# Performance work log

Measured on AMD Instinct MI355X. Metric: run time of the kernel, lower is better.

Reference implementation:

```python
import jax, jax.numpy as jnp
import numpy as np

B, T, N, IN = 16, 12, 2048, 1
HID, E_DIM, CHEB, HOR = 64, 10, 2, 12


def setup_inputs() -> dict:
    key = jax.random.key(0)
    ks = jax.random.split(key, 12)
    s = 0.1  # param scale to keep gates unsaturated
    return {
        "source": jax.random.normal(ks[0], (B, T, N, IN), jnp.float32),
        "node_embeddings": jax.random.normal(ks[1], (N, E_DIM), jnp.float32),
        "Wg0": jax.random.normal(ks[2], (E_DIM, CHEB, IN + HID, 2 * HID), jnp.float32) * s,
        "bg0": jax.random.normal(ks[3], (E_DIM, 2 * HID), jnp.float32) * s,
        "Wu0": jax.random.normal(ks[4], (E_DIM, CHEB, IN + HID, HID), jnp.float32) * s,
        "bu0": jax.random.normal(ks[5], (E_DIM, HID), jnp.float32) * s,
        "Wg1": jax.random.normal(ks[6], (E_DIM, CHEB, HID + HID, 2 * HID), jnp.float32) * s,
        "bg1": jax.random.normal(ks[7], (E_DIM, 2 * HID), jnp.float32) * s,
        "Wu1": jax.random.normal(ks[8], (E_DIM, CHEB, HID + HID, HID), jnp.float32) * s,
        "bu1": jax.random.normal(ks[9], (E_DIM, HID), jnp.float32) * s,
        "conv_w": jax.random.normal(ks[10], (HOR, HID), jnp.float32) * s,
        "conv_b": jax.random.normal(ks[11], (HOR,), jnp.float32) * s,
    }


def _cheb_supports(E, cheb_k):
    # softmax(relu(E E^T)) row-normalized adaptive adjacency + Chebyshev recursion
    S = jax.nn.softmax(jax.nn.relu(E @ E.T), axis=1)
    sup = [jnp.eye(E.shape[0], dtype=S.dtype), S]
    for _ in range(2, cheb_k):
        sup.append(2.0 * S @ sup[-1] - sup[-2])
    return jnp.stack(sup, axis=0)  # (K, N, N)


def _gcn(x, supports, weights, bias):
    # x: (B,N,C); weights: (N,K,C,O); bias: (N,O)
    x_g = jnp.einsum('knm,bmc->bnkc', supports, x)
    return jnp.einsum('bnki,nkio->bno', x_g, weights) + bias


def _layer(x_seq, supports, E, Wg, bg, Wu, bu, hid):
    # precompute node-adaptive weights/biases (constant across time)
    wg = jnp.einsum('nd,dkio->nkio', E, Wg)
    bgv = E @ bg
    wu = jnp.einsum('nd,dkio->nkio', E, Wu)
    buv = E @ bu

    def step(state, x_t):
        inp = jnp.concatenate([x_t, state], axis=-1)
        zr = jax.nn.sigmoid(_gcn(inp, supports, wg, bgv))
        z, r = jnp.split(zr, 2, axis=-1)
        cand = jnp.concatenate([x_t, z * state], axis=-1)
        hc = jnp.tanh(_gcn(cand, supports, wu, buv))
        h = r * state + (1.0 - r) * hc
        return h, h

    init = jnp.zeros((x_seq.shape[0], x_seq.shape[2], hid), dtype=x_seq.dtype)
    _, hs = jax.lax.scan(step, init, jnp.swapaxes(x_seq, 0, 1))  # (T,B,N,H)
    return jnp.swapaxes(hs, 0, 1)  # (B,T,N,H)


def reference(source, node_embeddings, Wg0, bg0, Wu0, bu0, Wg1, bg1, Wu1, bu1, conv_w, conv_b):
    supports = _cheb_supports(node_embeddings, CHEB)
    h1 = _layer(source, supports, node_embeddings, Wg0, bg0, Wu0, bu0, HID)
    h2 = _layer(h1, supports, node_embeddings, Wg1, bg1, Wu1, bu1, HID)
    last = h2[:, -1]  # (B,N,HID)
    # Conv2d(1, horizon, kernel=(1,HID)) on (B,1,N,HID) == per-node linear over HID
    out = jnp.einsum('bnc,hc->bhn', last, conv_w) + conv_b[None, :, None]
    return out  # (B, horizon, N)
```

## Files before the change

kernel.cpp:

```cpp
#include <hip/hip_runtime.h>
#include <hip/hip_bf16.h>


#define B_    16
#define T_    12
#define N_    2048
#define HID_  64
#define ED_   10
#define HOR_  12
#define BH    (B_*HID_)
#define BT    (B_*T_)
#define SL_   (N_*BH)

typedef __hip_bfloat16 bf16;
typedef __attribute__((ext_vector_type(8))) short short8;
typedef __attribute__((ext_vector_type(4))) float floatx4;

__device__ int            g_flag[64];
__device__ float          g_Ein[N_*ED_];
__device__ float          g_cwf[HOR_*HID_];
__device__ float          g_cbf[HOR_ + 4];
__device__ unsigned short g_Shi[N_*N_];
__device__ unsigned short g_Slo[N_*N_];
__device__ float          g_Wg0F[ED_*128*160];
__device__ float          g_Wu0F[ED_*64*160];
__device__ float          g_Wg1F[ED_*128*256];
__device__ float          g_Wu1F[ED_*64*256];
__device__ unsigned short g_Wg0H[ED_*128*160];
__device__ unsigned short g_Wu0H[ED_*64*160];
__device__ unsigned short g_Wg1H[ED_*128*256];
__device__ unsigned short g_Wu1H[ED_*64*256];
__device__ float          g_bgv0[N_*128];
__device__ float          g_buv0[N_*64];
__device__ float          g_bgv1[N_*128];
__device__ float          g_buv1[N_*64];
__device__ float          g_srcf[BT*N_];
__device__ unsigned short g_srcHi[BT*N_];
__device__ unsigned short g_srcLo[BT*N_];
__device__ float          g_Sx0[N_*BT];
__device__ float          g_h[2*SL_];
__device__ float          g_Sh[2*SL_];
__device__ float          g_zh[SL_];
__device__ float          g_rbuf[SL_];
__device__ unsigned short g_tmpTh[SL_];
__device__ unsigned short g_tmpTl[SL_];
__device__ unsigned short g_h2Th[SL_];
__device__ unsigned short g_h2Tl[SL_];

__device__ __forceinline__ float b2f(bf16 x){ return __bfloat162float(x); }
__device__ __forceinline__ bf16  f2b(float x){ return __float2bfloat16(x); }
__device__ __forceinline__ float bits2f(unsigned u) {
  union { float f; unsigned i; } c; c.i = u << 16; return c.f;
}
__device__ __forceinline__ float ldin(const void* p, size_t i, int isbf) {
  return isbf ? b2f(((const bf16*)p)[i]) : ((const float*)p)[i];
}
__device__ __forceinline__ void fma4(float4& a, float s, const float4& b) {
  a.x += s*b.x; a.y += s*b.y; a.z += s*b.z; a.w += s*b.w;
}

__global__ void k_detect(const void* __restrict__ E) {
  __shared__ int cnt;
  if (threadIdx.x == 0) cnt = 0;
  __syncthreads();
  const unsigned* w = (const unsigned*)E;
  int c = 0;
  for (int i = threadIdx.x; i < 4096; i += 256) {
    const unsigned e = (w[i] >> 7) & 0xFFu;
    if (e >= 0x6Eu && e <= 0x86u) ++c;
  }
  atomicAdd(&cnt, c);
  __syncthreads();
  if (threadIdx.x == 0) g_flag[0] = (cnt > 2048) ? 1 : 0;
}

__global__ void k_castE(const void* __restrict__ E) {
  const int i = blockIdx.x*256 + threadIdx.x;
  if (i < N_*ED_) g_Ein[i] = ldin(E, i, g_flag[0]);
}
__global__ void k_castsrc(const void* __restrict__ src) {
  const int i = blockIdx.x*256 + threadIdx.x;
  if (i < B_*T_*N_) g_srcf[i] = ldin(src, i, g_flag[0]);
}
__global__ void k_castc(const void* __restrict__ cw, const void* __restrict__ cb) {
  const int i = blockIdx.x*256 + threadIdx.x;
  const int f = g_flag[0];
  if (i < HOR_*HID_) g_cwf[i] = ldin(cw, i, f);
  if (i < HOR_)      g_cbf[i] = ldin(cb, i, f);
}

__global__ __launch_bounds__(256) void k_softmax_S() {
  bf16* Sh = (bf16*)g_Shi;
  bf16* Sl = (bf16*)g_Slo;
  const int n = blockIdx.x, tid = threadIdx.x;
  __shared__ float er[ED_];
  __shared__ float red[4];
  if (tid < ED_) er[tid] = g_Ein[n*ED_ + tid];
  __syncthreads();
  float e[ED_];
#pragma unroll
  for (int d = 0; d < ED_; ++d) e[d] = er[d];
  float v[8];
  float mx = 0.f;
#pragma unroll
  for (int j = 0; j < 8; ++j) {
    const int m = tid + j*256;
    float dot = 0.f;
#pragma unroll
    for (int d = 0; d < ED_; ++d) dot += e[d]*g_Ein[m*ED_ + d];
    v[j] = fmaxf(dot, 0.f);
    mx = fmaxf(mx, v[j]);
  }
  for (int o = 32; o; o >>= 1) mx = fmaxf(mx, __shfl_xor(mx, o, 64));
  if ((tid & 63) == 0) red[tid >> 6] = mx;
  __syncthreads();
  mx = fmaxf(fmaxf(red[0], red[1]), fmaxf(red[2], red[3]));
  __syncthreads();
  float sum = 0.f;
#pragma unroll
  for (int j = 0; j < 8; ++j) { v[j] = __expf(v[j] - mx); sum += v[j]; }
  for (int o = 32; o; o >>= 1) sum += __shfl_xor(sum, o, 64);
  if ((tid & 63) == 0) red[tid >> 6] = sum;
  __syncthreads();
  sum = red[0] + red[1] + red[2] + red[3];
  const float inv = 1.f / sum;
#pragma unroll
  for (int j = 0; j < 8; ++j) {
    const float sv = v[j]*inv;
    const size_t idx = (size_t)n*N_ + tid + j*256;
    const bf16 h = f2b(sv);
    Sh[idx] = h;
    Sl[idx] = f2b(sv - b2f(h));
  }
}

__global__ void k_splitSrc() {
  const int i = blockIdx.x*256 + threadIdx.x;
  if (i < BT*N_) {
    const float v = g_srcf[i];
    const bf16 h = f2b(v);
    ((bf16*)g_srcHi)[i] = h;
    ((bf16*)g_srcLo)[i] = f2b(v - b2f(h));
  }
}

__global__ __launch_bounds__(256) void k_trsp(int xsel, int dsel) {
  const float* X = (xsel == 0) ? g_h : (xsel == 1) ? (g_h + SL_) : g_zh;
  bf16* Th = (bf16*)((dsel == 0) ? g_tmpTh : g_h2Th);
  bf16* Tl = (bf16*)((dsel == 0) ? g_tmpTl : g_h2Tl);
  const int n0 = blockIdx.x * 64;
  const int c0 = blockIdx.y * 64;
  __shared__ float t[64][68];
  const int tid = threadIdx.x;
  {
    const int r = tid >> 2, q4 = (tid & 3) * 16;
    const float4* src = (const float4*)(X + (size_t)(n0 + r)*BH + c0 + q4);
#pragma unroll
    for (int u = 0; u < 4; ++u)
      *(float4*)&t[r][q4 + u*4] = src[u];
  }
  __syncthreads();
  {
    const int c = tid >> 2, sg = (tid & 3) * 16;
    bf16 hb[16], lb[16];
#pragma unroll
    for (int i = 0; i < 16; ++i) {
      const float v = t[sg + i][c];
      const bf16 h = f2b(v);
      hb[i] = h;
      lb[i] = f2b(v - b2f(h));
    }
    bf16* dh = Th + (size_t)(c0 + c)*N_ + n0 + sg;
    bf16* dl = Tl + (size_t)(c0 + c)*N_ + n0 + sg;
    *(uint4*)dh       = *(uint4*)&hb[0];
    *(uint4*)(dh + 8) = *(uint4*)&hb[8];
    *(uint4*)dl       = *(uint4*)&lb[0];
    *(uint4*)(dl + 8) = *(uint4*)&lb[8];
  }
}

template<int LAYER>
__global__ __launch_bounds__(256) void k_prepP(const void* __restrict__ Wb,
                                               int KIin, int KIP, int O,
                                               int wsel) {
  float* PF = (wsel == 0) ? g_Wg0F : (wsel == 1) ? g_Wu0F
            : (wsel == 2) ? g_Wg1F : g_Wu1F;
  bf16* PH = (bf16*)((wsel == 0) ? g_Wg0H : (wsel == 1) ? g_Wu0H
            : (wsel == 2) ? g_Wg1H : g_Wu1H);
  const int idx = blockIdx.x*256 + threadIdx.x;
  if (idx >= ED_*O*KIP) return;
  const int d = idx / (O*KIP), rem = idx - d*O*KIP;
  const int o = rem / KIP, kp = rem - o*KIP;
  int cheb, i; bool valid;
  if (LAYER == 0) {
    cheb = (kp >= 80) ? 1 : 0;
    const int local = kp - cheb*80;
    if (local < 64)       { i = local + 1; valid = true; }
    else if (local == 64) { i = 0;         valid = true; }
    else                  { i = 0;         valid = false; }
  } else {
    cheb = kp >> 7; i = kp & 127; valid = true;
  }
  float v = 0.f;
  if (valid) v = ldin(Wb, (size_t)((d*2 + cheb)*KIin + i)*O + o, g_flag[0]);
  const int kg = kp >> 2, e = kp & 3;
  const size_t pi = ((size_t)(o*(KIP/4) + kg)*ED_ + d)*4 + e;
  PF[pi] = v;
  PH[pi] = f2b(v);
}

__global__ __launch_bounds__(128) void k_matb(const void* __restrict__ bb,
                                              int O, int osel) {
  float* outv = (osel == 0) ? g_bgv0 : (osel == 1) ? g_buv0
              : (osel == 2) ? g_bgv1 : g_buv1;
  const int n = blockIdx.x, tid = threadIdx.x;
  if (tid >= O) return;
  const int f = g_flag[0];
  float acc = 0.f;
#pragma unroll
  for (int d = 0; d < ED_; ++d) acc += g_Ein[n*ED_ + d]*ldin(bb, d*O + tid, f);
  outv[n*O + tid] = acc;
}

__global__ __launch_bounds__(256) void k_gemmM(int x1, int c1, int ldc1,
                                               int x2, int c2, int ldc2,
                                               int split) {
  const bf16* Sh = (const bf16*)g_Shi;
  const bf16* Sl = (const bf16*)g_Slo;
  const int bm = blockIdx.x * 128;
  int bc = blockIdx.y * 64;
  int xs = x1, cs = c1, ldc = ldc1;
  if (bc >= split) { xs = x2; cs = c2; ldc = ldc2; bc -= split; }
  const bf16* Xh = (const bf16*)((xs == 0) ? g_tmpTh : (xs == 1) ? g_h2Th : g_srcHi);
  const bf16* Xl = (const bf16*)((xs == 0) ? g_tmpTl : (xs == 1) ? g_h2Tl : g_srcLo);
  float* C = (cs == 0) ? g_Sh : (cs == 1) ? (g_Sh + SL_) : g_Sx0;

  __shared__ __align__(16) bf16 Ah[128][72];
  __shared__ __align__(16) bf16 Al[128][72];
  __shared__ __align__(16) bf16 Bh[64][72];
  __shared__ __align__(16) bf16 Bl[64][72];
  const int tid = threadIdx.x;
  const int wave = tid >> 6, lane = tid & 63, q = lane >> 4, ln = lane & 15;
  const int wm = wave >> 1, wn = wave & 1;
  const int srow = tid >> 3, scol = (tid & 7) * 8;

  floatx4 acc[4][2];
#pragma unroll
  for (int mt = 0; mt < 4; ++mt)
#pragma unroll
    for (int nt = 0; nt < 2; ++nt) acc[mt][nt] = (floatx4){0.f,0.f,0.f,0.f};

  for (int mk = 0; mk < N_; mk += 64) {
#pragma unroll
    for (int i = 0; i < 4; ++i) {
      const int r = i*32 + srow;
      *(uint4*)&Ah[r][scol] = *(const uint4*)(Sh + (size_t)(bm + r)*N_ + mk + scol);
      *(uint4*)&Al[r][scol] = *(const uint4*)(Sl + (size_t)(bm + r)*N_ + mk + scol);
    }
#pragma unroll
    for (int i = 0; i < 2; ++i) {
      const int r = i*32 + srow;
      *(uint4*)&Bh[r][scol] = *(const uint4*)(Xh + (size_t)(bc + r)*N_ + mk + scol);
      *(uint4*)&Bl[r][scol] = *(const uint4*)(Xl + (size_t)(bc + r)*N_ + mk + scol);
    }
    __syncthreads();
#pragma unroll
    for (int ks = 0; ks < 64; ks += 32) {
      short8 ah[4], al[4], bh[2], bl[2];
#pragma unroll
      for (int mt = 0; mt < 4; ++mt) {
        ah[mt] = *(const short8*)&Ah[wm*64 + mt*16 + ln][ks + q*8];
        al[mt] = *(const short8*)&Al[wm*64 + mt*16 + ln][ks + q*8];
      }
#pragma unroll
      for (int nt = 0; nt < 2; ++nt) {
        bh[nt] = *(const short8*)&Bh[wn*32 + nt*16 + ln][ks + q*8];
        bl[nt] = *(const short8*)&Bl[wn*32 + nt*16 + ln][ks + q*8];
      }
#pragma unroll
      for (int mt = 0; mt < 4; ++mt)
#pragma unroll
        for (int nt = 0; nt < 2; ++nt) {
          acc[mt][nt] = __builtin_amdgcn_mfma_f32_16x16x32_bf16(ah[mt], bh[nt], acc[mt][nt], 0, 0, 0);
          acc[mt][nt] = __builtin_amdgcn_mfma_f32_16x16x32_bf16(al[mt], bh[nt], acc[mt][nt], 0, 0, 0);
          acc[mt][nt] = __builtin_amdgcn_mfma_f32_16x16x32_bf16(ah[mt], bl[nt], acc[mt][nt], 0, 0, 0);
        }
    }
    __syncthreads();
  }
#pragma unroll
  for (int mt = 0; mt < 4; ++mt)
#pragma unroll
    for (int nt = 0; nt < 2; ++nt)
#pragma unroll
      for (int r = 0; r < 4; ++r)
        C[(size_t)(bm + wm*64 + mt*16 + q*4 + r)*ldc + bc + wn*32 + nt*16 + ln] =
            acc[mt][nt][r];
}

template<int LAYER, int KIP, int KIPP>
__device__ __forceinline__ void build4(float (*xg)[KIPP],
                                       const float* p0, const float* p1,
                                       const float* p2, const float* p3,
                                       int n, int t, int tid) {
  constexpr int NQ = KIP/4;
  for (int idx = tid; idx < B_*NQ; idx += 256) {
    const int b = idx / NQ, k = (idx - b*NQ) * 4;
    float4 v = make_float4(0.f, 0.f, 0.f, 0.f);
    if (LAYER == 1) {
      const float* rg = (k < 64) ? p0 : (k < 128) ? p1 : (k < 192) ? p2 : p3;
      v = *(const float4*)(rg + (size_t)n*BH + b*64 + (k & 63));
    } else {
      if (k < 64)        v = *(const float4*)(p0 + (size_t)n*BH + b*64 + k);
      else if (k == 64)  v.x = p1[(size_t)(b*T_ + t)*N_ + n];
      else if (k >= 80 && k < 144)
                         v = *(const float4*)(p2 + (size_t)n*BH + b*64 + (k - 80));
      else if (k == 144) v.x = p3[(size_t)n*BT + b*T_ + t];
    }
    *(float4*)&xg[b][k] = v;
  }
}

template<int KIP>
__device__ __forceinline__ void merge_p2(const float* __restrict__ PF,
                                         const bf16* __restrict__ PH,
                                         const float* el0, const float* el1,
                                         int o, int kg, int isbf,
                                         float4& a0, float4& a1) {
  const size_t gbase = (size_t)(o*(KIP/4) + kg)*(ED_*4);
  if (isbf) {
    const uint4* g = (const uint4*)(PH + gbase);
#pragma unroll
    for (int i = 0; i < 5; ++i) {
      const uint4 w = g[i];
      const float f0 = bits2f(w.x & 0xFFFFu), f1 = bits2f(w.x >> 16);
      const float f2 = bits2f(w.y & 0xFFFFu), f3 = bits2f(w.y >> 16);
      const float f4 = bits2f(w.z & 0xFFFFu), f5 = bits2f(w.z >> 16);
      const float f6 = bits2f(w.w & 0xFFFFu), f7 = bits2f(w.w >> 16);
      const float e00 = el0[2*i], e01 = el0[2*i + 1];
      const float e10 = el1[2*i], e11 = el1[2*i + 1];
      a0.x += e00*f0; a0.y += e00*f1; a0.z += e00*f2; a0.w += e00*f3;
      a0.x += e01*f4; a0.y += e01*f5; a0.z += e01*f6; a0.w += e01*f7;
      a1.x += e10*f0; a1.y += e10*f1; a1.z += e10*f2; a1.w += e10*f3;
      a1.x += e11*f4; a1.y += e11*f5; a1.z += e11*f6; a1.w += e11*f7;
    }
  } else {
    const float4* g = (const float4*)(PF + gbase);
#pragma unroll
    for (int d = 0; d < ED_; ++d) {
      const float4 w = g[d];
      fma4(a0, el0[d], w);
      fma4(a1, el1[d], w);
    }
  }
}

template<int LAYER, int KIP>
__global__ __launch_bounds__(256, 2) void k_gateW2(int t) {
  constexpr int KIPP = KIP + 4;
  constexpr int O = 128;
  const float* PF = (LAYER == 0) ? g_Wg0F : g_Wg1F;
  const bf16*  PH = (const bf16*)((LAYER == 0) ? g_Wg0H : g_Wg1H);
  const float* bgv = (LAYER == 0) ? g_bgv0 : g_bgv1;
  const float* p0 = g_h;
  const float* p1 = (LAYER == 0) ? g_srcf : (g_h + SL_);
  const float* p2 = g_Sh;
  const float* p3 = (LAYER == 0) ? g_Sx0 : (g_Sh + SL_);
  const float* hstate = (LAYER == 0) ? g_h : (g_h + SL_);
  const int n0 = blockIdx.x, n1 = blockIdx.x + N_/2, tid = threadIdx.x;
  __shared__ float xg[2][B_][KIPP];
  __shared__ float wm[2][O][36];
  __shared__ float es[2][ED_];
  if (tid < ED_) es[0][tid] = g_Ein[n0*ED_ + tid];
  if (tid >= 32 && tid < 32 + ED_) es[1][tid - 32] = g_Ein[n1*ED_ + (tid - 32)];
  build4<LAYER, KIP, KIPP>(xg[0], p0, p1, p2, p3, n0, t, tid);
  build4<LAYER, KIP, KIPP>(xg[1], p0, p1, p2, p3, n1, t, tid);
  __syncthreads();
  const int isbf = g_flag[0];
  float el0[ED_], el1[ED_];
#pragma unroll
  for (int d = 0; d < ED_; ++d) { el0[d] = es[0][d]; el1[d] = es[1][d]; }

  const int b = tid >> 4, q = tid & 15;
  float ac0[8], ac1[8];
#pragma unroll
  for (int j = 0; j < 8; ++j) { ac0[j] = 0.f; ac1[j] = 0.f; }

  for (int k0 = 0; k0 < KIP; k0 += 32) {
#pragma unroll
    for (int i = 0; i < O*8/256; ++i) {
      const int idx = tid + i*256;
      const int o = idx >> 3, kq = idx & 7;
      float4 a0 = make_float4(0.f, 0.f, 0.f, 0.f);
      float4 a1 = make_float4(0.f, 0.f, 0.f, 0.f);
      merge_p2<KIP>(PF, PH, el0, el1, o, (k0 >> 2) + kq, isbf, a0, a1);
      *(float4*)&wm[0][o][kq*4] = a0;
      *(float4*)&wm[1][o][kq*4] = a1;
    }
    __syncthreads();
#pragma unroll
    for (int kq = 0; kq < 8; ++kq) {
      const float4 xv0 = *(const float4*)&xg[0][b][k0 + kq*4];
      const float4 xv1 = *(const float4*)&xg[1][b][k0 + kq*4];
#pragma unroll
      for (int j = 0; j < 8; ++j) {
        const float4 w0 = *(const float4*)&wm[0][q + 16*j][kq*4];
        const float4 w1 = *(const float4*)&wm[1][q + 16*j][kq*4];
        ac0[j] += xv0.x*w0.x + xv0.y*w0.y + xv0.z*w0.z + xv0.w*w0.w;
        ac1[j] += xv1.x*w1.x + xv1.y*w1.y + xv1.z*w1.z + xv1.w*w1.w;
      }
    }
    __syncthreads();
  }
#pragma unroll
  for (int j = 0; j < 8; ++j) {
    const int o = q + 16*j;
    {
      float s = ac0[j] + bgv[n0*128 + o];
      s = 1.f/(1.f + __expf(-s));
      if (o < HID_) {
        g_zh[(size_t)n0*BH + b*64 + o] = s*hstate[(size_t)n0*BH + b*64 + o];
      } else {
        g_rbuf[(size_t)n0*BH + b*64 + (o - HID_)] = s;
      }
    }
    {
      float s = ac1[j] + bgv[n1*128 + o];
      s = 1.f/(1.f + __expf(-s));
      if (o < HID_) {
        g_zh[(size_t)n1*BH + b*64 + o] = s*hstate[(size_t)n1*BH + b*64 + o];
      } else {
        g_rbuf[(size_t)n1*BH + b*64 + (o - HID_)] = s;
      }
    }
  }
}

template<int LAYER, int KIP>
__global__ __launch_bounds__(256, 2) void k_candW2f(int t) {
  constexpr int KIPP = KIP + 4;
  constexpr int O = 64;
  const float* PF = (LAYER == 0) ? g_Wu0F : g_Wu1F;
  const bf16*  PH = (const bf16*)((LAYER == 0) ? g_Wu0H : g_Wu1H);
  const float* buv = (LAYER == 0) ? g_buv0 : g_buv1;
  const float* p0 = (LAYER == 0) ? g_zh : g_h;
  const float* p1 = (LAYER == 0) ? g_srcf : g_zh;
  const float* p2 = (LAYER == 0) ? (g_Sh + SL_) : g_Sh;
  const float* p3 = (LAYER == 0) ? g_Sx0 : (g_Sh + SL_);
  float* hstate = (LAYER == 0) ? g_h : (g_h + SL_);
  const int n0 = blockIdx.x, n1 = blockIdx.x + N_/2, tid = threadIdx.x;
  __shared__ float xg[2][B_][KIPP];
  __shared__ float wm[2][O][36];
  __shared__ float es[2][ED_];
  if (tid < ED_) es[0][tid] = g_Ein[n0*ED_ + tid];
  if (tid >= 32 && tid < 32 + ED_) es[1][tid - 32] = g_Ein[n1*ED_ + (tid - 32)];
  build4<LAYER, KIP, KIPP>(xg[0], p0, p1, p2, p3, n0, t, tid);
  build4<LAYER, KIP, KIPP>(xg[1], p0, p1, p2, p3, n1, t, tid);
  __syncthreads();
  const int isbf = g_flag[0];
  float el0[ED_], el1[ED_];
#pragma unroll
  for (int d = 0; d < ED_; ++d) { el0[d] = es[0][d]; el1[d] = es[1][d]; }

  const int b = tid >> 4, q = tid & 15;
  float ac0[4], ac1[4];
#pragma unroll
  for (int j = 0; j < 4; ++j) { ac0[j] = 0.f; ac1[j] = 0.f; }

  for (int k0 = 0; k0 < KIP; k0 += 32) {
#pragma unroll
    for (int i = 0; i < O*8/256; ++i) {
      const int idx = tid + i*256;
      const int o = idx >> 3, kq = idx & 7;
      float4 a0 = make_float4(0.f, 0.f, 0.f, 0.f);
      float4 a1 = make_float4(0.f, 0.f, 0.f, 0.f);
      merge_p2<KIP>(PF, PH, el0, el1, o, (k0 >> 2) + kq, isbf, a0, a1);
      *(float4*)&wm[0][o][kq*4] = a0;
      *(float4*)&wm[1][o][kq*4] = a1;
    }
    __syncthreads();
#pragma unroll
    for (int kq = 0; kq < 8; ++kq) {
      const float4 xv0 = *(const float4*)&xg[0][b][k0 + kq*4];
      const float4 xv1 = *(const float4*)&xg[1][b][k0 + kq*4];
#pragma unroll
      for (int j = 0; j < 4; ++j) {
        const float4 w0 = *(const float4*)&wm[0][q + 16*j][kq*4];
        const float4 w1 = *(const float4*)&wm[1][q + 16*j][kq*4];
        ac0[j] += xv0.x*w0.x + xv0.y*w0.y + xv0.z*w0.z + xv0.w*w0.w;
        ac1[j] += xv1.x*w1.x + xv1.y*w1.y + xv1.z*w1.z + xv1.w*w1.w;
      }
    }
    __syncthreads();
  }
#pragma unroll
  for (int j = 0; j < 4; ++j) {
    const int o = q + 16*j;
    {
      const float hc = tanhf(ac0[j] + buv[n0*64 + o]);
      const float rr = g_rbuf[(size_t)n0*BH + b*64 + o];
      const float hold = hstate[(size_t)n0*BH + b*64 + o];
      hstate[(size_t)n0*BH + b*64 + o] = rr*hold + (1.f - rr)*hc;
    }
    {
      const float hc = tanhf(ac1[j] + buv[n1*64 + o]);
      const float rr = g_rbuf[(size_t)n1*BH + b*64 + o];
      const float hold = hstate[(size_t)n1*BH + b*64 + o];
      hstate[(size_t)n1*BH + b*64 + o] = rr*hold + (1.f - rr)*hc;
    }
  }
}

__global__ void k_zero_f(int sel) {
  float* p = (sel == 0) ? g_h : g_Sh;
  const int i = blockIdx.x*256 + threadIdx.x;
  if (i < 2*SL_) p[i] = 0.f;
}

__global__ __launch_bounds__(256) void k_conv(void* __restrict__ out) {
  const float* h2 = g_h + SL_;
  const int n = blockIdx.x, tid = threadIdx.x;
  __shared__ float hs[BH];
  for (int i = tid; i < BH; i += 256) hs[i] = h2[(size_t)n*BH + i];
  __syncthreads();
  const int isbf = g_flag[0];
  for (int i = tid; i < B_*HOR_; i += 256) {
    const int b = i / HOR_, hor = i - b*HOR_;
    float acc = g_cbf[hor];
#pragma unroll
    for (int c = 0; c < HID_; ++c) acc += hs[b*HID_ + c]*g_cwf[hor*HID_ + c];
    const size_t oi = (size_t)(b*HOR_ + hor)*N_ + n;
    if (isbf) ((bf16*)out)[oi] = f2b(acc);
    else      ((float*)out)[oi] = acc;
  }
}

extern "C" void kernel_launch(void* const* d_in, const int* in_sizes, int n_in,
                              void* d_out, int out_size, void* d_ws, size_t ws_size,
                              hipStream_t stream) {
  (void)out_size; (void)d_ws; (void)ws_size;

  static const long long cnt[12] = {
    393216,
    20480,
    166400,
    1280,
    83200,
    640,
    327680,
    1280,
    163840,
    640,
    768,
    12
  };
  const void* in[12];
  bool ok = (n_in == 12) && (in_sizes != nullptr) && (d_in != nullptr);
  if (ok) {
    long long mx = 0;
    for (int i = 0; i < 12; ++i) if ((long long)in_sizes[i] > mx) mx = in_sizes[i];
    long long scale = mx / 393216LL;
    if (scale != 1 && scale != 2 && scale != 4) ok = false;
    if (ok && scale*393216LL != mx) ok = false;
    bool used[12] = {false,false,false,false,false,false,false,false,false,false,false,false};
    for (int k = 0; k < 12 && ok; ++k) {
      int found = -1;
      for (int i = 0; i < 12; ++i)
        if (!used[i] && (long long)in_sizes[i] == cnt[k]*scale) { found = i; break; }
      if (found < 0) ok = false;
      else { used[found] = true; in[k] = d_in[found]; }
    }
  }
  if (!ok) for (int k = 0; k < 12; ++k) in[k] = d_in[k];

  const void* src = in[0];
  const void* E   = in[1];
  const void* Wg0 = in[2];
  const void* bg0 = in[3];
  const void* Wu0 = in[4];
  const void* bu0 = in[5];
  const void* Wg1 = in[6];
  const void* bg1 = in[7];
  const void* Wu1 = in[8];
  const void* bu1 = in[9];
  const void* cw  = in[10];
  const void* cb  = in[11];

  auto cdiv = [](int a, int b) { return (a + b - 1) / b; };

  k_detect<<<dim3(1), 256, 0, stream>>>(E);

  k_castE  <<<dim3(cdiv(N_*ED_, 256)), 256, 0, stream>>>(E);
  k_castsrc<<<dim3(cdiv(BT*N_, 256)),  256, 0, stream>>>(src);
  k_castc  <<<dim3(cdiv(HOR_*HID_, 256)), 256, 0, stream>>>(cw, cb);
  k_prepP<0><<<dim3(cdiv(ED_*128*160, 256)), 256, 0, stream>>>(Wg0, 65, 160, 128, 0);
  k_prepP<0><<<dim3(cdiv(ED_*64*160,  256)), 256, 0, stream>>>(Wu0, 65, 160, 64, 1);
  k_prepP<1><<<dim3(cdiv(ED_*128*256, 256)), 256, 0, stream>>>(Wg1, 128, 256, 128, 2);
  k_prepP<1><<<dim3(cdiv(ED_*64*256,  256)), 256, 0, stream>>>(Wu1, 128, 256, 64, 3);
  k_matb<<<dim3(N_), 128, 0, stream>>>(bg0, 128, 0);
  k_matb<<<dim3(N_), 128, 0, stream>>>(bu0, 64,  1);
  k_matb<<<dim3(N_), 128, 0, stream>>>(bg1, 128, 2);
  k_matb<<<dim3(N_), 128, 0, stream>>>(bu1, 64,  3);
  k_softmax_S<<<dim3(N_), 256, 0, stream>>>();
  k_splitSrc<<<dim3(cdiv(BT*N_, 256)), 256, 0, stream>>>();

  k_gemmM<<<dim3(N_/128, BT/64), 256, 0, stream>>>(2, 2, BT, 2, 2, BT, 1 << 30);

  k_zero_f<<<dim3((2*SL_ + 255)/256), 256, 0, stream>>>(0);
  k_zero_f<<<dim3((2*SL_ + 255)/256), 256, 0, stream>>>(1);

  k_gateW2<0,160><<<dim3(N_/2), 256, 0, stream>>>(0);
  k_candW2f<0,160><<<dim3(N_/2), 256, 0, stream>>>(0);
  k_trsp<<<dim3(N_/64, BH/64), 256, 0, stream>>>(0, 0);
  k_gemmM<<<dim3(N_/128, BH/64), 256, 0, stream>>>(0, 0, BH, 0, 0, BH, 1 << 30);
  k_gateW2<1,256><<<dim3(N_/2), 256, 0, stream>>>(0);
  k_candW2f<1,256><<<dim3(N_/2), 256, 0, stream>>>(0);
  k_trsp<<<dim3(N_/64, BH/64), 256, 0, stream>>>(1, 1);

  for (int t = 1; t < T_; ++t) {
    k_gateW2<0,160><<<dim3(N_/2), 256, 0, stream>>>(t);
    k_trsp<<<dim3(N_/64, BH/64), 256, 0, stream>>>(2, 0);
    k_gemmM<<<dim3(N_/128, BH/64), 256, 0, stream>>>(0, 1, BH, 0, 1, BH, 1 << 30);
    k_candW2f<0,160><<<dim3(N_/2), 256, 0, stream>>>(t);
    k_trsp<<<dim3(N_/64, BH/64), 256, 0, stream>>>(0, 0);
    k_gemmM<<<dim3(N_/128, 2*BH/64), 256, 0, stream>>>(0, 0, BH, 1, 1, BH, BH);
    k_gateW2<1,256><<<dim3(N_/2), 256, 0, stream>>>(t);
    k_trsp<<<dim3(N_/64, BH/64), 256, 0, stream>>>(2, 0);
    k_gemmM<<<dim3(N_/128, BH/64), 256, 0, stream>>>(0, 1, BH, 0, 1, BH, 1 << 30);
    k_candW2f<1,256><<<dim3(N_/2), 256, 0, stream>>>(t);
    k_trsp<<<dim3(N_/64, BH/64), 256, 0, stream>>>(1, 1);
  }

  k_conv<<<dim3(N_), 256, 0, stream>>>(d_out);
}
```

Measured before the change: 6.704 ms.

## Precompute per-node merged weights once instead of re-merging every timestep

Adds k_merge kernels that materialize the node-adaptive weights (E·W) for all nodes into large fp32 global buffers before the recurrence. The gate and candidate kernels then stream these precomputed weights instead of recomputing the 10-term embedding contraction at every timestep, and each block now handles one node instead of two. This trades repeated ALU work for much higher memory traffic, reading roughly 130 MB of weights per timestep, and adds about the same amount of global storage.

```diff
diff --git a/kernel.cpp b/kernel.cpp
--- a/kernel.cpp
+++ b/kernel.cpp
@@ -46,6 +46,10 @@
 __device__ unsigned short g_tmpTl[SL_];
 __device__ unsigned short g_h2Th[SL_];
 __device__ unsigned short g_h2Tl[SL_];
+__device__ float          g_Wg0M[(size_t)N_*128*160];
+__device__ float          g_Wu0M[(size_t)N_*64*160];
+__device__ float          g_Wg1M[(size_t)N_*128*256];
+__device__ float          g_Wu1M[(size_t)N_*64*256];
 
 __device__ __forceinline__ float b2f(bf16 x){ return __bfloat162float(x); }
 __device__ __forceinline__ bf16  f2b(float x){ return __float2bfloat16(x); }
@@ -222,6 +226,55 @@
   outv[n*O + tid] = acc;
 }
 
+template<int KIP>
+__device__ __forceinline__ float4 merge_p(const float* __restrict__ PF,
+                                          const bf16* __restrict__ PH,
+                                          const float* el, int o, int kg,
+                                          int isbf) {
+  float4 a4 = make_float4(0.f, 0.f, 0.f, 0.f);
+  const size_t gbase = (size_t)(o*(KIP/4) + kg)*(ED_*4);
+  if (isbf) {
+    const uint4* g = (const uint4*)(PH + gbase);
+#pragma unroll
+    for (int i = 0; i < 5; ++i) {
+      const uint4 w = g[i];
+      const float e0 = el[2*i], e1 = el[2*i + 1];
+      a4.x += e0*bits2f(w.x & 0xFFFFu); a4.y += e0*bits2f(w.x >> 16);
+      a4.z += e0*bits2f(w.y & 0xFFFFu); a4.w += e0*bits2f(w.y >> 16);
+      a4.x += e1*bits2f(w.z & 0xFFFFu); a4.y += e1*bits2f(w.z >> 16);
+      a4.z += e1*bits2f(w.w & 0xFFFFu); a4.w += e1*bits2f(w.w >> 16);
+    }
+  } else {
+    const float4* g = (const float4*)(PF + gbase);
+#pragma unroll
+    for (int d = 0; d < ED_; ++d)
+      fma4(a4, el[d], g[d]);
+  }
+  return a4;
+}
+
+template<int KIP>
+__global__ __launch_bounds__(256) void k_merge(int O, int wsel) {
+  const float* PF = (wsel == 0) ? g_Wg0F : (wsel == 1) ? g_Wu0F
+                  : (wsel == 2) ? g_Wg1F : g_Wu1F;
+  const bf16* PH = (const bf16*)((wsel == 0) ? g_Wg0H : (wsel == 1) ? g_Wu0H
+                  : (wsel == 2) ? g_Wg1H : g_Wu1H);
+  float* WM = (wsel == 0) ? g_Wg0M : (wsel == 1) ? g_Wu0M
+            : (wsel == 2) ? g_Wg1M : g_Wu1M;
+  const int n = blockIdx.x;
+  const int idx = blockIdx.y*256 + threadIdx.x;
+  __shared__ float es[ED_];
+  if (threadIdx.x < ED_) es[threadIdx.x] = g_Ein[n*ED_ + threadIdx.x];
+  __syncthreads();
+  if (idx >= O*(KIP/4)) return;
+  const int o = idx / (KIP/4), kg = idx - o*(KIP/4);
+  float el[ED_];
+#pragma unroll
+  for (int d = 0; d < ED_; ++d) el[d] = es[d];
+  const float4 a4 = merge_p<KIP>(PF, PH, el, o, kg, g_flag[0]);
+  *(float4*)&WM[((size_t)n*O + o)*KIP + kg*4] = a4;
+}
+
 __global__ __launch_bounds__(256) void k_gemmM(int x1, int c1, int ldc1,
                                                int x2, int c2, int ldc2,
                                                int split) {
@@ -321,93 +374,44 @@
   }
 }
 
-template<int KIP>
-__device__ __forceinline__ void merge_p2(const float* __restrict__ PF,
-                                         const bf16* __restrict__ PH,
-                                         const float* el0, const float* el1,
-                                         int o, int kg, int isbf,
-                                         float4& a0, float4& a1) {
-  const size_t gbase = (size_t)(o*(KIP/4) + kg)*(ED_*4);
-  if (isbf) {
-    const uint4* g = (const uint4*)(PH + gbase);
-#pragma unroll
-    for (int i = 0; i < 5; ++i) {
-      const uint4 w = g[i];
-      const float f0 = bits2f(w.x & 0xFFFFu), f1 = bits2f(w.x >> 16);
-      const float f2 = bits2f(w.y & 0xFFFFu), f3 = bits2f(w.y >> 16);
-      const float f4 = bits2f(w.z & 0xFFFFu), f5 = bits2f(w.z >> 16);
-      const float f6 = bits2f(w.w & 0xFFFFu), f7 = bits2f(w.w >> 16);
-      const float e00 = el0[2*i], e01 = el0[2*i + 1];
-      const float e10 = el1[2*i], e11 = el1[2*i + 1];
-      a0.x += e00*f0; a0.y += e00*f1; a0.z += e00*f2; a0.w += e00*f3;
-      a0.x += e01*f4; a0.y += e01*f5; a0.z += e01*f6; a0.w += e01*f7;
-      a1.x += e10*f0; a1.y += e10*f1; a1.z += e10*f2; a1.w += e10*f3;
-      a1.x += e11*f4; a1.y += e11*f5; a1.z += e11*f6; a1.w += e11*f7;
-    }
-  } else {
-    const float4* g = (const float4*)(PF + gbase);
-#pragma unroll
-    for (int d = 0; d < ED_; ++d) {
-      const float4 w = g[d];
-      fma4(a0, el0[d], w);
-      fma4(a1, el1[d], w);
-    }
-  }
-}
-
 template<int LAYER, int KIP>
-__global__ __launch_bounds__(256, 2) void k_gateW2(int t) {
+__global__ __launch_bounds__(256, 2) void k_gateWpm(int t) {
   constexpr int KIPP = KIP + 4;
   constexpr int O = 128;
-  const float* PF = (LAYER == 0) ? g_Wg0F : g_Wg1F;
-  const bf16*  PH = (const bf16*)((LAYER == 0) ? g_Wg0H : g_Wg1H);
+  const float* WM = (LAYER == 0) ? g_Wg0M : g_Wg1M;
   const float* bgv = (LAYER == 0) ? g_bgv0 : g_bgv1;
   const float* p0 = g_h;
   const float* p1 = (LAYER == 0) ? g_srcf : (g_h + SL_);
   const float* p2 = g_Sh;
   const float* p3 = (LAYER == 0) ? g_Sx0 : (g_Sh + SL_);
   const float* hstate = (LAYER == 0) ? g_h : (g_h + SL_);
-  const int n0 = blockIdx.x, n1 = blockIdx.x + N_/2, tid = threadIdx.x;
-  __shared__ float xg[2][B_][KIPP];
-  __shared__ float wm[2][O][36];
-  __shared__ float es[2][ED_];
-  if (tid < ED_) es[0][tid] = g_Ein[n0*ED_ + tid];
-  if (tid >= 32 && tid < 32 + ED_) es[1][tid - 32] = g_Ein[n1*ED_ + (tid - 32)];
-  build4<LAYER, KIP, KIPP>(xg[0], p0, p1, p2, p3, n0, t, tid);
-  build4<LAYER, KIP, KIPP>(xg[1], p0, p1, p2, p3, n1, t, tid);
-  __syncthreads();
-  const int isbf = g_flag[0];
-  float el0[ED_], el1[ED_];
-#pragma unroll
-  for (int d = 0; d < ED_; ++d) { el0[d] = es[0][d]; el1[d] = es[1][d]; }
-
+  const int n = blockIdx.x, tid = threadIdx.x;
+  __shared__ float xg[B_][KIPP];
+  __shared__ float wm[O][36];
+  build4<LAYER, KIP, KIPP>(xg, p0, p1, p2, p3, n, t, tid);
+
+  const float* WMn = WM + (size_t)n*O*KIP;
   const int b = tid >> 4, q = tid & 15;
-  float ac0[8], ac1[8];
-#pragma unroll
-  for (int j = 0; j < 8; ++j) { ac0[j] = 0.f; ac1[j] = 0.f; }
+  float acc[8];
+#pragma unroll
+  for (int j = 0; j < 8; ++j) acc[j] = 0.f;
 
   for (int k0 = 0; k0 < KIP; k0 += 32) {
 #pragma unroll
     for (int i = 0; i < O*8/256; ++i) {
       const int idx = tid + i*256;
       const int o = idx >> 3, kq = idx & 7;
-      float4 a0 = make_float4(0.f, 0.f, 0.f, 0.f);
-      float4 a1 = make_float4(0.f, 0.f, 0.f, 0.f);
-      merge_p2<KIP>(PF, PH, el0, el1, o, (k0 >> 2) + kq, isbf, a0, a1);
-      *(float4*)&wm[0][o][kq*4] = a0;
-      *(float4*)&wm[1][o][kq*4] = a1;
+      *(float4*)&wm[o][kq*4] =
+          *(const float4*)(WMn + (size_t)o*KIP + k0 + kq*4);
     }
     __syncthreads();
 #pragma unroll
     for (int kq = 0; kq < 8; ++kq) {
-      const float4 xv0 = *(const float4*)&xg[0][b][k0 + kq*4];
-      const float4 xv1 = *(const float4*)&xg[1][b][k0 + kq*4];
+      const float4 xv = *(const float4*)&xg[b][k0 + kq*4];
 #pragma unroll
       for (int j = 0; j < 8; ++j) {
-        const float4 w0 = *(const float4*)&wm[0][q + 16*j][kq*4];
-        const float4 w1 = *(const float4*)&wm[1][q + 16*j][kq*4];
-        ac0[j] += xv0.x*w0.x + xv0.y*w0.y + xv0.z*w0.z + xv0.w*w0.w;
-        ac1[j] += xv1.x*w1.x + xv1.y*w1.y + xv1.z*w1.z + xv1.w*w1.w;
+        const float4 wv = *(const float4*)&wm[q + 16*j][kq*4];
+        acc[j] += xv.x*wv.x + xv.y*wv.y + xv.z*wv.z + xv.w*wv.w;
       }
     }
     __syncthreads();
@@ -415,80 +419,54 @@
 #pragma unroll
   for (int j = 0; j < 8; ++j) {
     const int o = q + 16*j;
-    {
-      float s = ac0[j] + bgv[n0*128 + o];
-      s = 1.f/(1.f + __expf(-s));
-      if (o < HID_) {
-        g_zh[(size_t)n0*BH + b*64 + o] = s*hstate[(size_t)n0*BH + b*64 + o];
-      } else {
-        g_rbuf[(size_t)n0*BH + b*64 + (o - HID_)] = s;
-      }
-    }
-    {
-      float s = ac1[j] + bgv[n1*128 + o];
-      s = 1.f/(1.f + __expf(-s));
-      if (o < HID_) {
-        g_zh[(size_t)n1*BH + b*64 + o] = s*hstate[(size_t)n1*BH + b*64 + o];
-      } else {
-        g_rbuf[(size_t)n1*BH + b*64 + (o - HID_)] = s;
-      }
+    float s = acc[j] + bgv[n*128 + o];
+    s = 1.f/(1.f + __expf(-s));
+    if (o < HID_) {
+      g_zh[(size_t)n*BH + b*64 + o] = s*hstate[(size_t)n*BH + b*64 + o];
+    } else {
+      g_rbuf[(size_t)n*BH + b*64 + (o - HID_)] = s;
     }
   }
 }
 
 template<int LAYER, int KIP>
-__global__ __launch_bounds__(256, 2) void k_candW2f(int t) {
+__global__ __launch_bounds__(256, 2) void k_candWpm(int t) {
   constexpr int KIPP = KIP + 4;
   constexpr int O = 64;
-  const float* PF = (LAYER == 0) ? g_Wu0F : g_Wu1F;
-  const bf16*  PH = (const bf16*)((LAYER == 0) ? g_Wu0H : g_Wu1H);
+  const float* WM = (LAYER == 0) ? g_Wu0M : g_Wu1M;
   const float* buv = (LAYER == 0) ? g_buv0 : g_buv1;
   const float* p0 = (LAYER == 0) ? g_zh : g_h;
   const float* p1 = (LAYER == 0) ? g_srcf : g_zh;
   const float* p2 = (LAYER == 0) ? (g_Sh + SL_) : g_Sh;
   const float* p3 = (LAYER == 0) ? g_Sx0 : (g_Sh + SL_);
   float* hstate = (LAYER == 0) ? g_h : (g_h + SL_);
-  const int n0 = blockIdx.x, n1 = blockIdx.x + N_/2, tid = threadIdx.x;
-  __shared__ float xg[2][B_][KIPP];
-  __shared__ float wm[2][O][36];
-  __shared__ float es[2][ED_];
-  if (tid < ED_) es[0][tid] = g_Ein[n0*ED_ + tid];
-  if (tid >= 32 && tid < 32 + ED_) es[1][tid - 32] = g_Ein[n1*ED_ + (tid - 32)];
-  build4<LAYER, KIP, KIPP>(xg[0], p0, p1, p2, p3, n0, t, tid);
-  build4<LAYER, KIP, KIPP>(xg[1], p0, p1, p2, p3, n1, t, tid);
-  __syncthreads();
-  const int isbf = g_flag[0];
-  float el0[ED_], el1[ED_];
-#pragma unroll
-  for (int d = 0; d < ED_; ++d) { el0[d] = es[0][d]; el1[d] = es[1][d]; }
-
+  const int n = blockIdx.x, tid = threadIdx.x;
+  __shared__ float xg[B_][KIPP];
+  __shared__ float wm[O][36];
+  build4<LAYER, KIP, KIPP>(xg, p0, p1, p2, p3, n, t, tid);
+
+  const float* WMn = WM + (size_t)n*O*KIP;
   const int b = tid >> 4, q = tid & 15;
-  float ac0[4], ac1[4];
-#pragma unroll
-  for (int j = 0; j < 4; ++j) { ac0[j] = 0.f; ac1[j] = 0.f; }
+  float acc[4];
+#pragma unroll
+  for (int j = 0; j < 4; ++j) acc[j] = 0.f;
 
   for (int k0 = 0; k0 < KIP; k0 += 32) {
 #pragma unroll
     for (int i = 0; i < O*8/256; ++i) {
       const int idx = tid + i*256;
       const int o = idx >> 3, kq = idx & 7;
-      float4 a0 = make_float4(0.f, 0.f, 0.f, 0.f);
-      float4 a1 = make_float4(0.f, 0.f, 0.f, 0.f);
-      merge_p2<KIP>(PF, PH, el0, el1, o, (k0 >> 2) + kq, isbf, a0, a1);
-      *(float4*)&wm[0][o][kq*4] = a0;
-      *(float4*)&wm[1][o][kq*4] = a1;
+      *(float4*)&wm[o][kq*4] =
+          *(const float4*)(WMn + (size_t)o*KIP + k0 + kq*4);
     }
     __syncthreads();
 #pragma unroll
     for (int kq = 0; kq < 8; ++kq) {
-      const float4 xv0 = *(const float4*)&xg[0][b][k0 + kq*4];
-      const float4 xv1 = *(const float4*)&xg[1][b][k0 + kq*4];
+      const float4 xv = *(const float4*)&xg[b][k0 + kq*4];
 #pragma unroll
       for (int j = 0; j < 4; ++j) {
-        const float4 w0 = *(const float4*)&wm[0][q + 16*j][kq*4];
-        const float4 w1 = *(const float4*)&wm[1][q + 16*j][kq*4];
-        ac0[j] += xv0.x*w0.x + xv0.y*w0.y + xv0.z*w0.z + xv0.w*w0.w;
-        ac1[j] += xv1.x*w1.x + xv1.y*w1.y + xv1.z*w1.z + xv1.w*w1.w;
+        const float4 wv = *(const float4*)&wm[q + 16*j][kq*4];
+        acc[j] += xv.x*wv.x + xv.y*wv.y + xv.z*wv.z + xv.w*wv.w;
       }
     }
     __syncthreads();
@@ -496,18 +474,10 @@
 #pragma unroll
   for (int j = 0; j < 4; ++j) {
     const int o = q + 16*j;
-    {
-      const float hc = tanhf(ac0[j] + buv[n0*64 + o]);
-      const float rr = g_rbuf[(size_t)n0*BH + b*64 + o];
-      const float hold = hstate[(size_t)n0*BH + b*64 + o];
-      hstate[(size_t)n0*BH + b*64 + o] = rr*hold + (1.f - rr)*hc;
-    }
-    {
-      const float hc = tanhf(ac1[j] + buv[n1*64 + o]);
-      const float rr = g_rbuf[(size_t)n1*BH + b*64 + o];
-      const float hold = hstate[(size_t)n1*BH + b*64 + o];
-      hstate[(size_t)n1*BH + b*64 + o] = rr*hold + (1.f - rr)*hc;
-    }
+    const float hc = tanhf(acc[j] + buv[n*64 + o]);
+    const float rr = g_rbuf[(size_t)n*BH + b*64 + o];
+    const float hold = hstate[(size_t)n*BH + b*64 + o];
+    hstate[(size_t)n*BH + b*64 + o] = rr*hold + (1.f - rr)*hc;
   }
 }
 
@@ -541,18 +511,8 @@
   (void)out_size; (void)d_ws; (void)ws_size;
 
   static const long long cnt[12] = {
-    393216,
-    20480,
-    166400,
-    1280,
-    83200,
-    640,
-    327680,
-    1280,
-    163840,
-    640,
-    768,
-    12
+    393216, 20480, 166400, 1280, 83200, 640,
+    327680, 1280, 163840, 640, 768, 12
   };
   const void* in[12];
   bool ok = (n_in == 12) && (in_sizes != nullptr) && (d_in != nullptr);
@@ -604,30 +564,35 @@
   k_softmax_S<<<dim3(N_), 256, 0, stream>>>();
   k_splitSrc<<<dim3(cdiv(BT*N_, 256)), 256, 0, stream>>>();
 
+  k_merge<160><<<dim3(N_, 20), 256, 0, stream>>>(128, 0);
+  k_merge<160><<<dim3(N_, 10), 256, 0, stream>>>(64,  1);
+  k_merge<256><<<dim3(N_, 32), 256, 0, stream>>>(128, 2);
+  k_merge<256><<<dim3(N_, 16), 256, 0, stream>>>(64,  3);
+
   k_gemmM<<<dim3(N_/128, BT/64), 256, 0, stream>>>(2, 2, BT, 2, 2, BT, 1 << 30);
 
   k_zero_f<<<dim3((2*SL_ + 255)/256), 256, 0, stream>>>(0);
   k_zero_f<<<dim3((2*SL_ + 255)/256), 256, 0, stream>>>(1);
 
-  k_gateW2<0,160><<<dim3(N_/2), 256, 0, stream>>>(0);
-  k_candW2f<0,160><<<dim3(N_/2), 256, 0, stream>>>(0);
+  k_gateWpm<0,160><<<dim3(N_), 256, 0, stream>>>(0);
+  k_candWpm<0,160><<<dim3(N_), 256, 0, stream>>>(0);
   k_trsp<<<dim3(N_/64, BH/64), 256, 0, stream>>>(0, 0);
   k_gemmM<<<dim3(N_/128, BH/64), 256, 0, stream>>>(0, 0, BH, 0, 0, BH, 1 << 30);
-  k_gateW2<1,256><<<dim3(N_/2), 256, 0, stream>>>(0);
-  k_candW2f<1,256><<<dim3(N_/2), 256, 0, stream>>>(0);
+  k_gateWpm<1,256><<<dim3(N_), 256, 0, stream>>>(0);
+  k_candWpm<1,256><<<dim3(N_), 256, 0, stream>>>(0);
   k_trsp<<<dim3(N_/64, BH/64), 256, 0, stream>>>(1, 1);
 
   for (int t = 1; t < T_; ++t) {
-    k_gateW2<0,160><<<dim3(N_/2), 256, 0, stream>>>(t);
+    k_gateWpm<0,160><<<dim3(N_), 256, 0, stream>>>(t);
     k_trsp<<<dim3(N_/64, BH/64), 256, 0, stream>>>(2, 0);
     k_gemmM<<<dim3(N_/128, BH/64), 256, 0, stream>>>(0, 1, BH, 0, 1, BH, 1 << 30);
-    k_candW2f<0,160><<<dim3(N_/2), 256, 0, stream>>>(t);
+    k_candWpm<0,160><<<dim3(N_), 256, 0, stream>>>(t);
     k_trsp<<<dim3(N_/64, BH/64), 256, 0, stream>>>(0, 0);
     k_gemmM<<<dim3(N_/128, 2*BH/64), 256, 0, stream>>>(0, 0, BH, 1, 1, BH, BH);
-    k_gateW2<1,256><<<dim3(N_/2), 256, 0, stream>>>(t);
+    k_gateWpm<1,256><<<dim3(N_), 256, 0, stream>>>(t);
     k_trsp<<<dim3(N_/64, BH/64), 256, 0, stream>>>(2, 0);
     k_gemmM<<<dim3(N_/128, BH/64), 256, 0, stream>>>(0, 1, BH, 0, 1, BH, 1 << 30);
-    k_candW2f<1,256><<<dim3(N_/2), 256, 0, stream>>>(t);
+    k_candWpm<1,256><<<dim3(N_), 256, 0, stream>>>(t);
     k_trsp<<<dim3(N_/64, BH/64), 256, 0, stream>>>(1, 1);
   }
 
```

After: 6.273 ms. 1.07x faster.
